# Optimization experiments

Hardware: AMD Instinct MI355X
Metric: run time of the kernel (lower is better)

The kernel has to match this reference:

```python
import jax, jax.numpy as jnp
import numpy as np

B = 1024
H = 2048  # hidden_size
D = 2048  # input_size

def setup_inputs() -> dict:
    key = jax.random.key(0)
    k1, k2, k3, k4 = jax.random.split(key, 4)
    x = jax.random.normal(k1, (B, D), dtype=jnp.float32)
    h = jax.random.normal(k2, (B, H), dtype=jnp.float32)
    c = jax.random.normal(k3, (B, H), dtype=jnp.float32)
    W = jax.random.normal(k4, (D + H, 4 * H), dtype=jnp.float32) * 0.02
    return {"x": x, "h": h, "c": c, "W": W}

def reference(x, h, c, W):
    # merged = cat([x, h], dim=1); weighted = merged @ W
    merged = jnp.concatenate([x, h], axis=1)          # (B, D+H)
    weighted = merged @ W                             # (B, 4H)
    hid = W.shape[1] // 4
    c_f, c_i, c_g, c_o = jnp.split(weighted, 4, axis=1)
    c_new = c * jax.nn.sigmoid(c_f) + jax.nn.sigmoid(c_i) * jnp.tanh(c_g)
    h_new = jax.nn.sigmoid(c_o) * jnp.tanh(c_new)
    return h_new
```

## Files before the change

### kernel.cpp

```cpp
#include <hip/hip_runtime.h>

typedef __attribute__((ext_vector_type(4))) float          f32x4;
typedef __attribute__((ext_vector_type(8))) __bf16         bf16x8;
typedef __attribute__((ext_vector_type(8))) unsigned short u16x8;

#define B_  1024
#define D_  2048
#define H_  2048
#define K_  4096
#define N_  8192

__device__ __forceinline__ unsigned short f2bf_rne(float f) {
  unsigned u = __builtin_bit_cast(unsigned, f);
  u += 0x7fffu + ((u >> 16) & 1u);
  return (unsigned short)(u >> 16);
}

__device__ __forceinline__ float sigf(float x) {
  return 1.f / (1.f + __expf(-x));
}
__device__ __forceinline__ float tanhf_(float x) {
  float ax = fabsf(x);
  float t  = __expf(-2.f * ax);
  float r  = (1.f - t) / (1.f + t);
  return (x < 0.f) ? -r : r;
}

typedef const __attribute__((address_space(1))) unsigned int* gptr_t;
typedef __attribute__((address_space(3))) unsigned int*       lptr_t;
__device__ __forceinline__ void gl_lds16(const void* g, void* l) {
  __builtin_amdgcn_global_load_lds((gptr_t)g, (lptr_t)l, 16, 0, 0);
}

__global__ __launch_bounds__(256) void k_convert_merged(
    const float* __restrict__ x, const float* __restrict__ h,
    unsigned short* __restrict__ merged) {
  int tid = blockIdx.x * 256 + threadIdx.x;
  int e0  = tid * 8;
  int b   = e0 >> 12;
  int col = e0 & 4095;
  const float* src = (col < D_) ? (x + (size_t)b * D_ + col)
                                : (h + (size_t)b * H_ + (col - D_));
  f32x4 v0 = *(const f32x4*)src;
  f32x4 v1 = *(const f32x4*)(src + 4);
  u16x8 o;
  o[0] = f2bf_rne(v0[0]); o[1] = f2bf_rne(v0[1]);
  o[2] = f2bf_rne(v0[2]); o[3] = f2bf_rne(v0[3]);
  o[4] = f2bf_rne(v1[0]); o[5] = f2bf_rne(v1[1]);
  o[6] = f2bf_rne(v1[2]); o[7] = f2bf_rne(v1[3]);
  *(u16x8*)(merged + e0) = o;
}

__global__ __launch_bounds__(256) void k_transpose_w(
    const float* __restrict__ W, unsigned short* __restrict__ Wt) {
  __shared__ float lt[64 * 64];
  char* lbase = (char*)lt;
  const int t  = threadIdx.x;
  const int n0 = blockIdx.x * 64;
  const int k0 = blockIdx.y * 64;
#pragma unroll
  for (int i = 0; i < 4; ++i) {
    int kk = (t >> 4) + i * 16;
    int nn = (t & 15) * 4;
    f32x4 v = *(const f32x4*)&W[(size_t)(k0 + kk) * N_ + n0 + nn];
    int by = (kk * 256 + nn * 4) ^ (((kk >> 3) & 7) << 4);
    *(f32x4*)(lbase + by) = v;
  }
  __syncthreads();
#pragma unroll
  for (int i = 0; i < 2; ++i) {
    int n  = (t >> 3) + i * 32;
    int kc = (t & 7) * 8;
    u16x8 o;
#pragma unroll
    for (int j = 0; j < 8; ++j) {
      int k  = kc + j;
      int by = (k * 256 + n * 4) ^ (((k >> 3) & 7) << 4);
      o[j] = f2bf_rne(*(const float*)(lbase + by));
    }
    *(u16x8*)&Wt[(size_t)(n0 + n) * K_ + k0 + kc] = o;
  }
}

#define TM 128
#define TN 128
#define TK 64

__global__ __launch_bounds__(256) void k_gemm(
    const unsigned short* __restrict__ A,
    const unsigned short* __restrict__ Bt,
    float* __restrict__ C) {
  __shared__ unsigned short As[TM * TK];
  __shared__ unsigned short Bs[TN * TK];
  const int t    = threadIdx.x;
  const int bx   = blockIdx.x;
  const int by   = blockIdx.y;
  const int wid  = t >> 6;
  const int lane = t & 63;
  const int wr   = wid >> 1, wc = wid & 1;
  const int ln15 = lane & 15, kq = lane >> 4;

  const int srow  = t >> 3;
  const int scolb = (t & 7) * 16;

  const char* gA = (const char*)A + (size_t)(by * TM + srow) * (K_ * 2) + scolb;
  const char* gB = (const char*)Bt + (size_t)(bx * TN + srow) * (K_ * 2) + scolb;
  char* lA = (char*)As + srow * (TK * 2) + scolb;
  char* lB = (char*)Bs + srow * (TK * 2) + scolb;

  f32x4 acc[4][4] = {};

  for (int kt = 0; kt < K_ / TK; ++kt) {
    const int gofs = kt * (TK * 2);
#pragma unroll
    for (int i = 0; i < 4; ++i) {
      gl_lds16(gA + (size_t)(i * 32) * (K_ * 2) + gofs, lA + i * 32 * (TK * 2));
      gl_lds16(gB + (size_t)(i * 32) * (K_ * 2) + gofs, lB + i * 32 * (TK * 2));
    }
    __syncthreads();
#pragma unroll
    for (int ks = 0; ks < 2; ++ks) {
      bf16x8 a[4], b[4];
#pragma unroll
      for (int mi = 0; mi < 4; ++mi)
        a[mi] = *(const bf16x8*)((const char*)As +
                 (wr * 64 + mi * 16 + ln15) * (TK * 2) + ks * 64 + kq * 16);
#pragma unroll
      for (int ni = 0; ni < 4; ++ni)
        b[ni] = *(const bf16x8*)((const char*)Bs +
                 (wc * 64 + ni * 16 + ln15) * (TK * 2) + ks * 64 + kq * 16);
#pragma unroll
      for (int mi = 0; mi < 4; ++mi)
#pragma unroll
        for (int ni = 0; ni < 4; ++ni)
          acc[mi][ni] = __builtin_amdgcn_mfma_f32_16x16x32_bf16(
              a[mi], b[ni], acc[mi][ni], 0, 0, 0);
    }
    __syncthreads();
  }

  const int crow0 = by * TM + wr * 64 + kq * 4;
  const int ccol0 = bx * TN + wc * 64 + ln15;
#pragma unroll
  for (int mi = 0; mi < 4; ++mi)
#pragma unroll
    for (int ni = 0; ni < 4; ++ni)
#pragma unroll
      for (int r = 0; r < 4; ++r)
        C[(size_t)(crow0 + mi * 16 + r) * N_ + ccol0 + ni * 16] = acc[mi][ni][r];
}

__global__ __launch_bounds__(256) void k_gates(
    const float* __restrict__ wsum, const float* __restrict__ c,
    float* __restrict__ out) {
  int tid = blockIdx.x * 256 + threadIdx.x;
  int b   = tid >> 9;
  int j   = (tid & 511) * 4;
  const float* base = wsum + (size_t)b * N_;
  f32x4 f  = *(const f32x4*)(base + j);
  f32x4 ii = *(const f32x4*)(base + H_ + j);
  f32x4 g  = *(const f32x4*)(base + 2 * H_ + j);
  f32x4 o  = *(const f32x4*)(base + 3 * H_ + j);
  f32x4 cc = *(const f32x4*)&c[(size_t)b * H_ + j];
  f32x4 r;
#pragma unroll
  for (int q = 0; q < 4; ++q) {
    float cn = cc[q] * sigf(f[q]) + sigf(ii[q]) * tanhf_(g[q]);
    r[q] = sigf(o[q]) * tanhf_(cn);
  }
  *(f32x4*)&out[(size_t)b * H_ + j] = r;
}

extern "C" void kernel_launch(void* const* d_in, const int* in_sizes, int n_in,
                              void* d_out, int out_size, void* d_ws, size_t ws_size,
                              hipStream_t stream) {
  (void)in_sizes; (void)n_in; (void)out_size; (void)ws_size;
  const float* x = (const float*)d_in[0];
  const float* h = (const float*)d_in[1];
  const float* c = (const float*)d_in[2];
  const float* W = (const float*)d_in[3];
  float* out = (float*)d_out;

  char* ws = (char*)d_ws;
  unsigned short* merged = (unsigned short*)ws;
  unsigned short* Wt     = (unsigned short*)(ws + (size_t)8  * 1024 * 1024);
  float*          wsum   = (float*)(ws + (size_t)72 * 1024 * 1024);

  k_convert_merged<<<2048, 256, 0, stream>>>(x, h, merged);
  k_transpose_w<<<dim3(128, 64), 256, 0, stream>>>(W, Wt);
  k_gemm<<<dim3(N_ / TN, B_ / TM), 256, 0, stream>>>(merged, Wt, wsum);
  k_gates<<<2048, 256, 0, stream>>>(wsum, c, out);
}
```

Baseline: 322.5 us.

## Fuse LSTM gate epilogue into GEMM by interleaving gate columns of W

The weight transpose now interleaves the four gate columns so that each group of four adjacent output columns holds f,i,g,o for one hidden unit. The GEMM epilogue gathers the four gates with lane shuffles, applies the LSTM cell math, and writes h_new directly. This removes the separate gates kernel and the 32 MB fp32 intermediate write and read. In exchange, only one lane in four does the stores, and they are scattered scalar writes.

```diff
diff --git a/kernel.cpp b/kernel.cpp
--- a/kernel.cpp
+++ b/kernel.cpp
@@ -55,30 +55,33 @@
     const float* __restrict__ W, unsigned short* __restrict__ Wt) {
   __shared__ float lt[64 * 64];
   char* lbase = (char*)lt;
-  const int t  = threadIdx.x;
-  const int n0 = blockIdx.x * 64;
-  const int k0 = blockIdx.y * 64;
+  const int t   = threadIdx.x;
+  const int g   = blockIdx.x & 3;
+  const int jb  = blockIdx.x >> 2;
+  const int n0s = g * 2048 + jb * 64;
+  const int k0  = blockIdx.y * 64;
 #pragma unroll
   for (int i = 0; i < 4; ++i) {
     int kk = (t >> 4) + i * 16;
     int nn = (t & 15) * 4;
-    f32x4 v = *(const f32x4*)&W[(size_t)(k0 + kk) * N_ + n0 + nn];
+    f32x4 v = *(const f32x4*)&W[(size_t)(k0 + kk) * N_ + n0s + nn];
     int by = (kk * 256 + nn * 4) ^ (((kk >> 3) & 7) << 4);
     *(f32x4*)(lbase + by) = v;
   }
   __syncthreads();
 #pragma unroll
   for (int i = 0; i < 2; ++i) {
-    int n  = (t >> 3) + i * 32;
+    int jl = (t >> 3) + i * 32;
     int kc = (t & 7) * 8;
     u16x8 o;
 #pragma unroll
-    for (int j = 0; j < 8; ++j) {
-      int k  = kc + j;
-      int by = (k * 256 + n * 4) ^ (((k >> 3) & 7) << 4);
-      o[j] = f2bf_rne(*(const float*)(lbase + by));
+    for (int jj = 0; jj < 8; ++jj) {
+      int k  = kc + jj;
+      int by = (k * 256 + jl * 4) ^ (((k >> 3) & 7) << 4);
+      o[jj] = f2bf_rne(*(const float*)(lbase + by));
     }
-    *(u16x8*)&Wt[(size_t)(n0 + n) * K_ + k0 + kc] = o;
+    int nrow = 4 * (jb * 64 + jl) + g;
+    *(u16x8*)&Wt[(size_t)nrow * K_ + k0 + kc] = o;
   }
 }
 
@@ -89,7 +92,8 @@
 __global__ __launch_bounds__(256) void k_gemm(
     const unsigned short* __restrict__ A,
     const unsigned short* __restrict__ Bt,
-    float* __restrict__ C) {
+    const float* __restrict__ c,
+    float* __restrict__ out) {
   __shared__ unsigned short As[TM * TK];
   __shared__ unsigned short Bs[TN * TK];
   const int t    = threadIdx.x;
@@ -140,35 +144,27 @@
   }
 
   const int crow0 = by * TM + wr * 64 + kq * 4;
-  const int ccol0 = bx * TN + wc * 64 + ln15;
+  const int s     = ln15 & 3;
+  const int q     = ln15 >> 2;
+  const int jbase = bx * 32 + wc * 16 + q;
 #pragma unroll
   for (int mi = 0; mi < 4; ++mi)
 #pragma unroll
     for (int ni = 0; ni < 4; ++ni)
 #pragma unroll
-      for (int r = 0; r < 4; ++r)
-        C[(size_t)(crow0 + mi * 16 + r) * N_ + ccol0 + ni * 16] = acc[mi][ni][r];
-}
-
-__global__ __launch_bounds__(256) void k_gates(
-    const float* __restrict__ wsum, const float* __restrict__ c,
-    float* __restrict__ out) {
-  int tid = blockIdx.x * 256 + threadIdx.x;
-  int b   = tid >> 9;
-  int j   = (tid & 511) * 4;
-  const float* base = wsum + (size_t)b * N_;
-  f32x4 f  = *(const f32x4*)(base + j);
-  f32x4 ii = *(const f32x4*)(base + H_ + j);
-  f32x4 g  = *(const f32x4*)(base + 2 * H_ + j);
-  f32x4 o  = *(const f32x4*)(base + 3 * H_ + j);
-  f32x4 cc = *(const f32x4*)&c[(size_t)b * H_ + j];
-  f32x4 r;
-#pragma unroll
-  for (int q = 0; q < 4; ++q) {
-    float cn = cc[q] * sigf(f[q]) + sigf(ii[q]) * tanhf_(g[q]);
-    r[q] = sigf(o[q]) * tanhf_(cn);
-  }
-  *(f32x4*)&out[(size_t)b * H_ + j] = r;
+      for (int r = 0; r < 4; ++r) {
+        float v  = acc[mi][ni][r];
+        float v1 = __shfl_xor(v, 1);
+        float v2 = __shfl_xor(v, 2);
+        float v3 = __shfl_xor(v, 3);
+        if (s == 0) {
+          int row = crow0 + mi * 16 + r;
+          int j   = jbase + ni * 4;
+          float cv = c[(size_t)row * H_ + j];
+          float cn = cv * sigf(v) + sigf(v1) * tanhf_(v2);
+          out[(size_t)row * H_ + j] = sigf(v3) * tanhf_(cn);
+        }
+      }
 }
 
 extern "C" void kernel_launch(void* const* d_in, const int* in_sizes, int n_in,
@@ -184,10 +180,8 @@
   char* ws = (char*)d_ws;
   unsigned short* merged = (unsigned short*)ws;
   unsigned short* Wt     = (unsigned short*)(ws + (size_t)8  * 1024 * 1024);
-  float*          wsum   = (float*)(ws + (size_t)72 * 1024 * 1024);
 
   k_convert_merged<<<2048, 256, 0, stream>>>(x, h, merged);
   k_transpose_w<<<dim3(128, 64), 256, 0, stream>>>(W, Wt);
-  k_gemm<<<dim3(N_ / TN, B_ / TM), 256, 0, stream>>>(merged, Wt, wsum);
-  k_gates<<<2048, 256, 0, stream>>>(wsum, c, out);
+  k_gemm<<<dim3(N_ / TN, B_ / TM), 256, 0, stream>>>(merged, Wt, c, out);
 }
```

Measured after the change: 343.0 us. 6.4% more time.
